# Kernel optimization log

Measured on AMD Instinct MI355X. Metric: run time of the kernel, lower is better.

## Reference

```python
import jax, jax.numpy as jnp
import numpy as np


def gcn_conv(x, W, b, src, dst, w, num_nodes):
    """PyG GCNConv: out = D^{-1/2} (A + I) D^{-1/2} (x @ W) + b, edge weights w."""
    xw = x @ W  # [BN, out_dim]
    # degree with self-loop weight 1.0, accumulated at target nodes
    deg = jax.ops.segment_sum(w, dst, num_segments=num_nodes) + 1.0  # [BN]
    dinv = jax.lax.rsqrt(deg)
    norm = dinv[src] * w * dinv[dst]  # [E]
    agg = jax.ops.segment_sum(xw[src] * norm[:, None], dst, num_segments=num_nodes)
    agg = agg + xw * (dinv * dinv)[:, None]  # self-loop contribution
    return agg + b


def setup_inputs() -> dict:
    key = jax.random.key(0)
    ks = jax.random.split(key, 10)
    BN, E, D = 100000, 1600000, 128
    return {
        "x": jax.random.normal(ks[0], (BN, D), dtype=jnp.float32),
        "edge_index": jax.random.randint(ks[1], (2, E), 0, BN, dtype=jnp.int64),
        "B": 8,
        "N": 12500,
        "causal_edge_index": jax.random.randint(ks[2], (2, 16), 0, BN, dtype=jnp.int64),
        "edge_weight": jax.random.uniform(ks[3], (E,), dtype=jnp.float32),
        "causal_edge_weight": jax.random.uniform(ks[4], (16,), dtype=jnp.float32),
        "W1": jax.random.normal(ks[5], (D, D), dtype=jnp.float32) * (1.0 / np.sqrt(D)),
        "b1": jnp.zeros((D,), dtype=jnp.float32),
        "W2": jax.random.normal(ks[6], (D, D), dtype=jnp.float32) * (1.0 / np.sqrt(D)),
        "b2": jnp.zeros((D,), dtype=jnp.float32),
        "Wres": jax.random.normal(ks[7], (D, D), dtype=jnp.float32) * (1.0 / np.sqrt(D)),
        "bres": jnp.zeros((D,), dtype=jnp.float32),
    }


def reference(x, edge_index, B, N, causal_edge_index, edge_weight,
              causal_edge_weight, W1, b1, W2, b2, Wres, bres):
    BN = B * N
    src, dst = edge_index[0], edge_index[1]
    # layer 1: GCNConv -> gelu (dropout is identity in eval)
    h = gcn_conv(x, W1, b1, src, dst, edge_weight, BN)  # [BN, hidden]
    h = jax.nn.gelu(h, approximate=False)
    # residual: 0.3 * Linear(x)
    h = h + 0.3 * (x @ Wres + bres)
    # layer 2: GCNConv -> gelu
    out = gcn_conv(h, W2, b2, src, dst, edge_weight, BN)
    return jax.nn.gelu(out, approximate=False)
```

## Files before the change

kernel.cpp:

```cpp
#include <hip/hip_runtime.h>
#include <math.h>

#define DIM 128
#define SCAN_CHUNK 4096

typedef __attribute__((ext_vector_type(8))) short short8;
typedef __attribute__((ext_vector_type(4))) float f32x4;

__device__ __forceinline__ float gelu_exact(float v) {
    return 0.5f * v * (1.0f + erff(v * 0.70710678118654752f));
}

__device__ __forceinline__ unsigned short f2bf(float f) {
    unsigned int u = __float_as_uint(f);
    return (unsigned short)((u + 0x7FFFu + ((u >> 16) & 1u)) >> 16);
}
__device__ __forceinline__ float bf_lo(unsigned int v) { return __uint_as_float(v << 16); }
__device__ __forceinline__ float bf_hi(unsigned int v) { return __uint_as_float(v & 0xFFFF0000u); }


__global__ void deg_cnt_kernel(const int* __restrict__ dst,
                               const float* __restrict__ w,
                               unsigned long long* __restrict__ packed,
                               int* __restrict__ rank, int E) {
    int e = blockIdx.x * blockDim.x + threadIdx.x;
    if (e >= E) return;
    int d = dst[e];
    unsigned long long inc =
        (1ull << 32) | (unsigned long long)(unsigned int)(w[e] * 67108864.0f);
    unsigned long long old = atomicAdd(&packed[d], inc);
    rank[e] = (int)(old >> 32);
}


__global__ __launch_bounds__(256) void wt3_kernel(const float* __restrict__ W1,
                                                  const float* __restrict__ Wres,
                                                  const float* __restrict__ W2,
                                                  unsigned short* __restrict__ Wt1,
                                                  unsigned short* __restrict__ Wtr,
                                                  unsigned short* __restrict__ Wt2) {
    int b = blockIdx.x;
    const float* W = (b < 64) ? W1 : (b < 128) ? Wres : W2;
    unsigned short* Wt = (b < 64) ? Wt1 : (b < 128) ? Wtr : Wt2;
    int idx = (b & 63) * 256 + threadIdx.x;
    int r = idx >> 7, c = idx & 127;
    Wt[c * 128 + r] = f2bf(W[idx]);
}


template <int MODE>
__device__ __forceinline__ void gemm_body(const float* __restrict__ X,
                                          const unsigned short* __restrict__ Wt,
                                          const float* __restrict__ bias,
                                          unsigned short* __restrict__ outb,
                                          float* __restrict__ Bf, int bid, int BN) {
    int tid = threadIdx.x;
    int w = tid >> 6, l = tid & 63;
    int l15 = l & 15, kg = l >> 4;
    int row0 = bid * 64 + w * 16;

    int rowA = row0 + l15;
    if (rowA > BN - 1) rowA = BN - 1;
    const float* ap = X + (size_t)rowA * 128 + kg * 8;

    f32x4 acc[8];
#pragma unroll
    for (int nt = 0; nt < 8; nt++) acc[nt] = (f32x4){0.f, 0.f, 0.f, 0.f};

#pragma unroll
    for (int ks = 0; ks < 4; ks++) {
        float4 a0 = *(const float4*)(ap + ks * 32);
        float4 a1 = *(const float4*)(ap + ks * 32 + 4);
        short8 aF;
        aF[0] = (short)f2bf(a0.x); aF[1] = (short)f2bf(a0.y);
        aF[2] = (short)f2bf(a0.z); aF[3] = (short)f2bf(a0.w);
        aF[4] = (short)f2bf(a1.x); aF[5] = (short)f2bf(a1.y);
        aF[6] = (short)f2bf(a1.z); aF[7] = (short)f2bf(a1.w);
#pragma unroll
        for (int nt = 0; nt < 8; nt++) {
            int colB = nt * 16 + l15;
            uint4 bu = *(const uint4*)(Wt + (size_t)colB * 128 + ks * 32 + kg * 8);
            short8 bF = __builtin_bit_cast(short8, bu);
            acc[nt] = __builtin_amdgcn_mfma_f32_16x16x32_bf16(aF, bF, acc[nt], 0, 0, 0);
        }
    }

#pragma unroll
    for (int nt = 0; nt < 8; nt++) {
        int col = nt * 16 + l15;
#pragma unroll
        for (int r = 0; r < 4; r++) {
            int row = row0 + kg * 4 + r;
            if (row >= BN) continue;
            size_t idx = (size_t)row * 128 + col;
            if (MODE == 0) {
                outb[idx] = f2bf(acc[nt][r]);
            } else {
                Bf[idx] = 0.3f * (acc[nt][r] + bias[col]);
            }
        }
    }
}

template <int MODE>
__global__ __launch_bounds__(256) void mfma_gemm_kernel(const float* __restrict__ X,
                                                        const unsigned short* __restrict__ Wt,
                                                        const float* __restrict__ bias,
                                                        unsigned short* __restrict__ outb,
                                                        float* __restrict__ Bf, int BN) {
    gemm_body<MODE>(X, Wt, bias, outb, Bf, blockIdx.x, BN);
}

__global__ __launch_bounds__(256) void gemm2x_kernel(const float* __restrict__ x,
                                                     const unsigned short* __restrict__ Wt1,
                                                     const unsigned short* __restrict__ Wtr,
                                                     const float* __restrict__ bres,
                                                     unsigned short* __restrict__ Ab,
                                                     float* __restrict__ Bf,
                                                     int BN, int gB) {
    int b = blockIdx.x;
    if (b < gB) gemm_body<0>(x, Wt1, nullptr, Ab, nullptr, b, BN);
    else        gemm_body<2>(x, Wtr, bres, nullptr, Bf, b - gB, BN);
}


__global__ __launch_bounds__(256) void scanAD_kernel(const unsigned long long* __restrict__ packed,
                                                     float* __restrict__ dinvf,
                                                     int* __restrict__ cnt,
                                                     int* __restrict__ partials, int BN) {
    int tid = threadIdx.x;
    int base = blockIdx.x * SCAN_CHUNK;
    int sum = 0;
#pragma unroll
    for (int i = 0; i < 16; i++) {
        int ii = base + i * 256 + tid;
        if (ii < BN) {
            unsigned long long v = packed[ii];
            int c = (int)(v >> 32);
            cnt[ii] = c;
            dinvf[ii] = rsqrtf((float)(unsigned int)(v & 0xFFFFFFFFu) * (1.0f / 67108864.0f) + 1.0f);
            sum += c;
        }
    }
    __shared__ int lds[4];
#pragma unroll
    for (int off = 32; off; off >>= 1) sum += __shfl_down(sum, off, 64);
    if ((tid & 63) == 0) lds[tid >> 6] = sum;
    __syncthreads();
    if (tid == 0) partials[blockIdx.x] = lds[0] + lds[1] + lds[2] + lds[3];
}

__global__ __launch_bounds__(256) void scanB_kernel(int* __restrict__ partials, int nblk) {
    __shared__ int lds[256];
    int tid = threadIdx.x;
    int v = (tid < nblk) ? partials[tid] : 0;
    lds[tid] = v;
    __syncthreads();
#pragma unroll
    for (int off = 1; off < 256; off <<= 1) {
        int t = (tid >= off) ? lds[tid - off] : 0;
        __syncthreads();
        lds[tid] += t;
        __syncthreads();
    }
    if (tid < nblk) partials[tid] = lds[tid] - v;
}

__global__ __launch_bounds__(256) void scanC_kernel(const int* __restrict__ cnt,
                                                    const int* __restrict__ partials,
                                                    int* __restrict__ ptr, int BN) {
    __shared__ int lds[256];
    int tid = threadIdx.x;
    int base = blockIdx.x * SCAN_CHUNK;
    int idx0 = base + tid * 16;
    int v[16];
    int tsum = 0;
#pragma unroll
    for (int j = 0; j < 16; j++) {
        int ii = idx0 + j;
        v[j] = (ii < BN) ? cnt[ii] : 0;
        tsum += v[j];
    }
    lds[tid] = tsum;
    __syncthreads();
#pragma unroll
    for (int off = 1; off < 256; off <<= 1) {
        int t = (tid >= off) ? lds[tid - off] : 0;
        __syncthreads();
        lds[tid] += t;
        __syncthreads();
    }
    int excl = lds[tid] - tsum + partials[blockIdx.x];
#pragma unroll
    for (int j = 0; j < 16; j++) {
        int ii = idx0 + j;
        if (ii < BN) ptr[ii] = excl;
        excl += v[j];
    }
}

__global__ void fill_kernel(const int* __restrict__ ei, const float* __restrict__ w,
                            const int* __restrict__ rank, const int* __restrict__ ptr,
                            const float* __restrict__ dinvf,
                            int2* __restrict__ csr, int E) {
    int e = blockIdx.x * blockDim.x + threadIdx.x;
    if (e >= E) return;
    int s = ei[e];
    int d = ei[(size_t)E + e];
    int pos = ptr[d] + rank[e];
    float nrm = dinvf[s] * w[e] * dinvf[d];
    csr[pos] = make_int2(s, __float_as_int(nrm));
}


template <int ACCMODE>
__global__ __launch_bounds__(256) void agg_kernel(const unsigned short* __restrict__ XWb,
                                                  const float* __restrict__ dinvf,
                                                  const int* __restrict__ ptr,
                                                  const int* __restrict__ cnt,
                                                  const int2* __restrict__ csr,
                                                  const float* __restrict__ bias,
                                                  float* __restrict__ out, int BN) {
    int h = threadIdx.x >> 5;
    int lane = threadIdx.x & 31;
    int n = blockIdx.x * 8 + h;
    if (n >= BN) return;
    int beg = ptr[n];
    int endv = beg + cnt[n];

    float4 a0 = make_float4(0.f, 0.f, 0.f, 0.f);
    float4 a1 = make_float4(0.f, 0.f, 0.f, 0.f);
    float4 a2 = make_float4(0.f, 0.f, 0.f, 0.f);
    float4 a3 = make_float4(0.f, 0.f, 0.f, 0.f);
    int i = beg;
    for (; i + 3 < endv; i += 4) {
        int2 e0 = csr[i], e1 = csr[i + 1], e2 = csr[i + 2], e3 = csr[i + 3];
        uint2 r0 = *(const uint2*)(XWb + (size_t)e0.x * 128 + lane * 4);
        uint2 r1 = *(const uint2*)(XWb + (size_t)e1.x * 128 + lane * 4);
        uint2 r2 = *(const uint2*)(XWb + (size_t)e2.x * 128 + lane * 4);
        uint2 r3 = *(const uint2*)(XWb + (size_t)e3.x * 128 + lane * 4);
        float n0 = __int_as_float(e0.y), n1 = __int_as_float(e1.y);
        float n2 = __int_as_float(e2.y), n3 = __int_as_float(e3.y);
        a0.x += n0 * bf_lo(r0.x); a0.y += n0 * bf_hi(r0.x);
        a0.z += n0 * bf_lo(r0.y); a0.w += n0 * bf_hi(r0.y);
        a1.x += n1 * bf_lo(r1.x); a1.y += n1 * bf_hi(r1.x);
        a1.z += n1 * bf_lo(r1.y); a1.w += n1 * bf_hi(r1.y);
        a2.x += n2 * bf_lo(r2.x); a2.y += n2 * bf_hi(r2.x);
        a2.z += n2 * bf_lo(r2.y); a2.w += n2 * bf_hi(r2.y);
        a3.x += n3 * bf_lo(r3.x); a3.y += n3 * bf_hi(r3.x);
        a3.z += n3 * bf_lo(r3.y); a3.w += n3 * bf_hi(r3.y);
    }
    for (; i < endv; i++) {
        int2 e0 = csr[i];
        uint2 r0 = *(const uint2*)(XWb + (size_t)e0.x * 128 + lane * 4);
        float n0 = __int_as_float(e0.y);
        a0.x += n0 * bf_lo(r0.x); a0.y += n0 * bf_hi(r0.x);
        a0.z += n0 * bf_lo(r0.y); a0.w += n0 * bf_hi(r0.y);
    }
    float dn = dinvf[n];
    float sl = dn * dn;
    uint2 rs = *(const uint2*)(XWb + (size_t)n * 128 + lane * 4);
    float4 bb = ((const float4*)bias)[lane];
    float4 o;
    o.x = gelu_exact(a0.x + a1.x + a2.x + a3.x + sl * bf_lo(rs.x) + bb.x);
    o.y = gelu_exact(a0.y + a1.y + a2.y + a3.y + sl * bf_hi(rs.x) + bb.y);
    o.z = gelu_exact(a0.z + a1.z + a2.z + a3.z + sl * bf_lo(rs.y) + bb.z);
    o.w = gelu_exact(a0.w + a1.w + a2.w + a3.w + sl * bf_hi(rs.y) + bb.w);
    float4* op = (float4*)(out + (size_t)n * 128) + lane;
    if (ACCMODE == 1) {
        float4 prev = *op;
        o.x += prev.x; o.y += prev.y; o.z += prev.z; o.w += prev.w;
    }
    *op = o;
}


extern "C" void kernel_launch(void* const* d_in, const int* in_sizes, int n_in,
                              void* d_out, int out_size, void* d_ws, size_t ws_size,
                              hipStream_t stream) {
    const float* x = (const float*)d_in[0];
    const int* ei = (const int*)d_in[1];
    const float* w = (const float*)d_in[5];
    const float* W1 = (const float*)d_in[7];
    const float* b1 = (const float*)d_in[8];
    const float* W2 = (const float*)d_in[9];
    const float* b2 = (const float*)d_in[10];
    const float* Wres = (const float*)d_in[11];
    const float* bres = (const float*)d_in[12];

    const int BN = in_sizes[0] / DIM;
    const int E = in_sizes[1] / 2;
    const int NBLK = (BN + SCAN_CHUNK - 1) / SCAN_CHUNK;

    char* p = (char*)d_ws;
    unsigned short* Ab = (unsigned short*)p;         p += (size_t)BN * DIM * 2;
    unsigned long long* packed = (unsigned long long*)p;  p += (size_t)BN * 8;
    float* dinvf = (float*)p;          p += (size_t)BN * 4;
    int* cnt = (int*)p;                p += (size_t)BN * 4;
    int* ptr = (int*)p;                p += (size_t)BN * 4;
    int* partials = (int*)p;           p += 1024;
    unsigned short* Wt1 = (unsigned short*)p;   p += 128 * 128 * 2;
    unsigned short* Wtr = (unsigned short*)p;   p += 128 * 128 * 2;
    unsigned short* Wt2 = (unsigned short*)p;   p += 128 * 128 * 2;
    int* rank = (int*)p;               p += (size_t)E * 4;
    int2* csr = (int2*)p;              p += (size_t)E * 8;

    float* Bf = (float*)d_out;

    const int* dst32 = ei + E;

    hipMemsetAsync(packed, 0, (size_t)BN * 8, stream);

    int tE = (E + 255) / 256;
    int gB = (BN + 63) / 64;
    int aggBlocks = (BN + 7) / 8;

    deg_cnt_kernel<<<tE, 256, 0, stream>>>(dst32, w, packed, rank, E);
    wt3_kernel<<<192, 256, 0, stream>>>(W1, Wres, W2, Wt1, Wtr, Wt2);

    gemm2x_kernel<<<2 * gB, 256, 0, stream>>>(x, Wt1, Wtr, bres, Ab, Bf, BN, gB);

    scanAD_kernel<<<NBLK, 256, 0, stream>>>(packed, dinvf, cnt, partials, BN);
    scanB_kernel<<<1, 256, 0, stream>>>(partials, NBLK);
    scanC_kernel<<<NBLK, 256, 0, stream>>>(cnt, partials, ptr, BN);
    fill_kernel<<<tE, 256, 0, stream>>>(ei, w, rank, ptr, dinvf, csr, E);

    agg_kernel<1><<<aggBlocks, 256, 0, stream>>>(Ab, dinvf, ptr, cnt, csr, b1, Bf, BN);

    mfma_gemm_kernel<0><<<gB, 256, 0, stream>>>(Bf, Wt2, nullptr, Ab, nullptr, BN);
    agg_kernel<0><<<aggBlocks, 256, 0, stream>>>(Ab, dinvf, ptr, cnt, csr, b2, (float*)d_out, BN);
}
```

Baseline: 501.5 us.

## Make GEMMs persistent with register-resident weights and prefetched A tiles

The dense GEMM kernels become persistent grid-stride kernels. Each block loads the full bf16 weight fragments into registers once and loops over row tiles, prefetching the next tile's A rows while the current tile runs its MFMAs. This removes repeated weight loads from L2 per tile and the per-block launch overhead. In exchange it uses many more registers per thread, which can reduce occupancy and latency hiding.

```diff
diff --git a/kernel.cpp b/kernel.cpp
--- a/kernel.cpp
+++ b/kernel.cpp
@@ -3,6 +3,7 @@
 
 #define DIM 128
 #define SCAN_CHUNK 4096
+#define NB_HALF 256
 
 typedef __attribute__((ext_vector_type(8))) short short8;
 typedef __attribute__((ext_vector_type(4))) float f32x4;
@@ -49,78 +50,107 @@
 
 
 template <int MODE>
-__device__ __forceinline__ void gemm_body(const float* __restrict__ X,
-                                          const unsigned short* __restrict__ Wt,
-                                          const float* __restrict__ bias,
-                                          unsigned short* __restrict__ outb,
-                                          float* __restrict__ Bf, int bid, int BN) {
+__device__ __forceinline__ void gemm_breg_body(const float* __restrict__ X,
+                                               const unsigned short* __restrict__ Wt,
+                                               const float* __restrict__ bias,
+                                               unsigned short* __restrict__ outb,
+                                               float* __restrict__ Bf,
+                                               int BN, int t0, int tStride) {
     int tid = threadIdx.x;
-    int w = tid >> 6, l = tid & 63;
+    int wv = tid >> 6, l = tid & 63;
     int l15 = l & 15, kg = l >> 4;
-    int row0 = bid * 64 + w * 16;
-
-    int rowA = row0 + l15;
-    if (rowA > BN - 1) rowA = BN - 1;
-    const float* ap = X + (size_t)rowA * 128 + kg * 8;
-
-    f32x4 acc[8];
-#pragma unroll
-    for (int nt = 0; nt < 8; nt++) acc[nt] = (f32x4){0.f, 0.f, 0.f, 0.f};
-
-#pragma unroll
-    for (int ks = 0; ks < 4; ks++) {
-        float4 a0 = *(const float4*)(ap + ks * 32);
-        float4 a1 = *(const float4*)(ap + ks * 32 + 4);
-        short8 aF;
-        aF[0] = (short)f2bf(a0.x); aF[1] = (short)f2bf(a0.y);
-        aF[2] = (short)f2bf(a0.z); aF[3] = (short)f2bf(a0.w);
-        aF[4] = (short)f2bf(a1.x); aF[5] = (short)f2bf(a1.y);
-        aF[6] = (short)f2bf(a1.z); aF[7] = (short)f2bf(a1.w);
+
+    uint4 b[4][8];
+#pragma unroll
+    for (int ks = 0; ks < 4; ks++)
+#pragma unroll
+        for (int nt = 0; nt < 8; nt++)
+            b[ks][nt] = *(const uint4*)(Wt + (size_t)(nt * 16 + l15) * 128 + ks * 32 + kg * 8);
+
+    float bias_r[8];
+    if (MODE == 2) {
+#pragma unroll
+        for (int nt = 0; nt < 8; nt++) bias_r[nt] = bias[nt * 16 + l15];
+    }
+
+    int nTiles = (BN + 63) / 64;
+
+    float4 aRaw[8];
+    {
+        int rowA = t0 * 64 + wv * 16 + l15;
+        if (rowA > BN - 1) rowA = BN - 1;
+        const float* ap = X + (size_t)rowA * 128 + kg * 8;
+#pragma unroll
+        for (int ks = 0; ks < 4; ks++) {
+            aRaw[2 * ks] = *(const float4*)(ap + ks * 32);
+            aRaw[2 * ks + 1] = *(const float4*)(ap + ks * 32 + 4);
+        }
+    }
+
+    for (int t = t0; t < nTiles; t += tStride) {
+        short8 aF[4];
+#pragma unroll
+        for (int ks = 0; ks < 4; ks++) {
+            float4 a0 = aRaw[2 * ks], a1 = aRaw[2 * ks + 1];
+            aF[ks][0] = (short)f2bf(a0.x); aF[ks][1] = (short)f2bf(a0.y);
+            aF[ks][2] = (short)f2bf(a0.z); aF[ks][3] = (short)f2bf(a0.w);
+            aF[ks][4] = (short)f2bf(a1.x); aF[ks][5] = (short)f2bf(a1.y);
+            aF[ks][6] = (short)f2bf(a1.z); aF[ks][7] = (short)f2bf(a1.w);
+        }
+        int tn = t + tStride;
+        if (tn < nTiles) {
+            int rowA = tn * 64 + wv * 16 + l15;
+            if (rowA > BN - 1) rowA = BN - 1;
+            const float* ap = X + (size_t)rowA * 128 + kg * 8;
+#pragma unroll
+            for (int ks = 0; ks < 4; ks++) {
+                aRaw[2 * ks] = *(const float4*)(ap + ks * 32);
+                aRaw[2 * ks + 1] = *(const float4*)(ap + ks * 32 + 4);
+            }
+        }
+
+        f32x4 acc[8];
+#pragma unroll
+        for (int nt = 0; nt < 8; nt++) acc[nt] = (f32x4){0.f, 0.f, 0.f, 0.f};
+#pragma unroll
+        for (int ks = 0; ks < 4; ks++)
+#pragma unroll
+            for (int nt = 0; nt < 8; nt++)
+                acc[nt] = __builtin_amdgcn_mfma_f32_16x16x32_bf16(
+                    aF[ks], __builtin_bit_cast(short8, b[ks][nt]), acc[nt], 0, 0, 0);
+
+        int row0 = t * 64 + wv * 16;
 #pragma unroll
         for (int nt = 0; nt < 8; nt++) {
-            int colB = nt * 16 + l15;
-            uint4 bu = *(const uint4*)(Wt + (size_t)colB * 128 + ks * 32 + kg * 8);
-            short8 bF = __builtin_bit_cast(short8, bu);
-            acc[nt] = __builtin_amdgcn_mfma_f32_16x16x32_bf16(aF, bF, acc[nt], 0, 0, 0);
-        }
-    }
-
-#pragma unroll
-    for (int nt = 0; nt < 8; nt++) {
-        int col = nt * 16 + l15;
-#pragma unroll
-        for (int r = 0; r < 4; r++) {
-            int row = row0 + kg * 4 + r;
-            if (row >= BN) continue;
-            size_t idx = (size_t)row * 128 + col;
-            if (MODE == 0) {
-                outb[idx] = f2bf(acc[nt][r]);
-            } else {
-                Bf[idx] = 0.3f * (acc[nt][r] + bias[col]);
+            int col = nt * 16 + l15;
+#pragma unroll
+            for (int r = 0; r < 4; r++) {
+                int row = row0 + kg * 4 + r;
+                if (row >= BN) continue;
+                size_t idx = (size_t)row * 128 + col;
+                if (MODE == 0) outb[idx] = f2bf(acc[nt][r]);
+                else           Bf[idx] = 0.3f * (acc[nt][r] + bias_r[nt]);
             }
         }
     }
 }
 
-template <int MODE>
-__global__ __launch_bounds__(256) void mfma_gemm_kernel(const float* __restrict__ X,
+__global__ __launch_bounds__(256, 2) void gemm2x_kernel(const float* __restrict__ x,
+                                                        const unsigned short* __restrict__ Wt1,
+                                                        const unsigned short* __restrict__ Wtr,
+                                                        const float* __restrict__ bres,
+                                                        unsigned short* __restrict__ Ab,
+                                                        float* __restrict__ Bf, int BN) {
+    int b = blockIdx.x;
+    if (b < NB_HALF) gemm_breg_body<0>(x, Wt1, nullptr, Ab, nullptr, BN, b, NB_HALF);
+    else             gemm_breg_body<2>(x, Wtr, bres, nullptr, Bf, BN, b - NB_HALF, NB_HALF);
+}
+
+__global__ __launch_bounds__(256, 2) void gemm1x_kernel(const float* __restrict__ X,
                                                         const unsigned short* __restrict__ Wt,
-                                                        const float* __restrict__ bias,
                                                         unsigned short* __restrict__ outb,
-                                                        float* __restrict__ Bf, int BN) {
-    gemm_body<MODE>(X, Wt, bias, outb, Bf, blockIdx.x, BN);
-}
-
-__global__ __launch_bounds__(256) void gemm2x_kernel(const float* __restrict__ x,
-                                                     const unsigned short* __restrict__ Wt1,
-                                                     const unsigned short* __restrict__ Wtr,
-                                                     const float* __restrict__ bres,
-                                                     unsigned short* __restrict__ Ab,
-                                                     float* __restrict__ Bf,
-                                                     int BN, int gB) {
-    int b = blockIdx.x;
-    if (b < gB) gemm_body<0>(x, Wt1, nullptr, Ab, nullptr, b, BN);
-    else        gemm_body<2>(x, Wtr, bres, nullptr, Bf, b - gB, BN);
+                                                        int BN) {
+    gemm_breg_body<0>(X, Wt, nullptr, outb, nullptr, BN, blockIdx.x, 2 * NB_HALF);
 }
 
 
@@ -312,13 +342,12 @@
     hipMemsetAsync(packed, 0, (size_t)BN * 8, stream);
 
     int tE = (E + 255) / 256;
-    int gB = (BN + 63) / 64;
     int aggBlocks = (BN + 7) / 8;
 
     deg_cnt_kernel<<<tE, 256, 0, stream>>>(dst32, w, packed, rank, E);
     wt3_kernel<<<192, 256, 0, stream>>>(W1, Wres, W2, Wt1, Wtr, Wt2);
 
-    gemm2x_kernel<<<2 * gB, 256, 0, stream>>>(x, Wt1, Wtr, bres, Ab, Bf, BN, gB);
+    gemm2x_kernel<<<2 * NB_HALF, 256, 0, stream>>>(x, Wt1, Wtr, bres, Ab, Bf, BN);
 
     scanAD_kernel<<<NBLK, 256, 0, stream>>>(packed, dinvf, cnt, partials, BN);
     scanB_kernel<<<1, 256, 0, stream>>>(partials, NBLK);
@@ -327,6 +356,6 @@
 
     agg_kernel<1><<<aggBlocks, 256, 0, stream>>>(Ab, dinvf, ptr, cnt, csr, b1, Bf, BN);
 
-    mfma_gemm_kernel<0><<<gB, 256, 0, stream>>>(Bf, Wt2, nullptr, Ab, nullptr, BN);
+    gemm1x_kernel<<<2 * NB_HALF, 256, 0, stream>>>(Bf, Wt2, Ab, BN);
     agg_kernel<0><<<aggBlocks, 256, 0, stream>>>(Ab, dinvf, ptr, cnt, csr, b2, (float*)d_out, BN);
 }
```

New measurement: 450.7 us. 10.1% less time.
